# Performance work log

Hardware: AMD Instinct MI355X
Metric: run time of the kernel (lower is better)

Reference implementation:

```python
import jax, jax.numpy as jnp
import numpy as np

B, N, C = 4, 2048, 768
H = 12
DH = C // H
HID = int(C * 4.0)
SCALE = DH ** -0.5
EPS = 1e-5


def layernorm(x, g, b):
    mu = jnp.mean(x, axis=-1, keepdims=True)
    var = jnp.var(x, axis=-1, keepdims=True)
    return (x - mu) * jax.lax.rsqrt(var + EPS) * g + b


def setup_inputs() -> dict:
    key = jax.random.key(0)
    ks = jax.random.split(key, 10)
    s = lambda fan_in: 1.0 / np.sqrt(fan_in)
    return {
        "x": jax.random.normal(ks[0], (B, N, C), dtype=jnp.float32),
        "ln1_g": jnp.ones((C,), jnp.float32),
        "ln1_b": jnp.zeros((C,), jnp.float32),
        "w_qkv": jax.random.uniform(ks[1], (C, 3 * C), jnp.float32, -s(C), s(C)),
        "w_proj": jax.random.uniform(ks[2], (C, C), jnp.float32, -s(C), s(C)),
        "b_proj": jnp.zeros((C,), jnp.float32),
        "ln2_g": jnp.ones((C,), jnp.float32),
        "ln2_b": jnp.zeros((C,), jnp.float32),
        "w_fc1": jax.random.uniform(ks[3], (C, HID), jnp.float32, -s(C), s(C)),
        "b_fc1": jnp.zeros((HID,), jnp.float32),
        "w_fc2": jax.random.uniform(ks[4], (HID, C), jnp.float32, -s(HID), s(HID)),
        "b_fc2": jnp.zeros((C,), jnp.float32),
    }


def reference(x, ln1_g, ln1_b, w_qkv, w_proj, b_proj, ln2_g, ln2_b, w_fc1, b_fc1, w_fc2, b_fc2):
    # --- attention branch ---
    h = layernorm(x, ln1_g, ln1_b)                       # [B,N,C]
    qkv = (h @ w_qkv).reshape(B, N, 3, H, DH)
    q = qkv[:, :, 0].transpose(0, 2, 1, 3)               # [B,H,N,DH]
    k = qkv[:, :, 1].transpose(0, 2, 1, 3)
    v = qkv[:, :, 2].transpose(0, 2, 1, 3)
    attn = jnp.einsum('bhnd,bhmd->bhnm', q, k) * SCALE   # [B,H,N,N]
    attn = jax.nn.softmax(attn, axis=-1)
    y = jnp.einsum('bhnm,bhmd->bhnd', attn, v)           # [B,H,N,DH]
    y = y.transpose(0, 2, 1, 3).reshape(B, N, C)
    y = y @ w_proj + b_proj
    x = x + y
    # --- MLP branch ---
    h = layernorm(x, ln2_g, ln2_b)
    h = jax.nn.gelu(h @ w_fc1 + b_fc1, approximate=False)
    h = h @ w_fc2 + b_fc2
    return x + h
```

## Files before the change

kernel.cpp:

```cpp
#include <hip/hip_runtime.h>
#include <stdint.h>

#define DEV __device__ __forceinline__

typedef __attribute__((ext_vector_type(8))) short bf16x8;
typedef __attribute__((ext_vector_type(4))) float f32x4;
typedef __attribute__((ext_vector_type(4))) short s16x4;

DEV short f2bf(float f) {
    union { float f; unsigned u; } v; v.f = f;
    unsigned r = v.u + 0x7fffu + ((v.u >> 16) & 1u);
    return (short)(r >> 16);
}

DEV uint32_t cvtpk(float lo, float hi) {
    uint32_t r;
    asm("v_cvt_pk_bf16_f32 %0, %1, %2" : "=v"(r) : "v"(lo), "v"(hi));
    return r;
}

typedef const unsigned int __attribute__((address_space(1)))* gp1;
typedef unsigned int __attribute__((address_space(3)))* lp3;

DEV void gload16(const void* g, void* l) {
    __builtin_amdgcn_global_load_lds((gp1)g, (lp3)l, 16, 0, 0);
}

DEV void wait4_barrier() { asm volatile("s_waitcnt vmcnt(4)\ns_barrier" ::: "memory"); }
DEV void wait2_barrier() { asm volatile("s_waitcnt vmcnt(2)\ns_barrier" ::: "memory"); }
DEV void wait0_barrier() { asm volatile("s_waitcnt vmcnt(0)\ns_barrier" ::: "memory"); }

__global__ __launch_bounds__(256) void tcvt(
    const float* __restrict__ W, short* __restrict__ WT, int K, int N)
{
    __shared__ float t[32][33];
    int n0 = blockIdx.x * 32, k0 = blockIdx.y * 32;
    int tx = threadIdx.x & 31, ty = threadIdx.x >> 5;
#pragma unroll
    for (int i = 0; i < 32; i += 8)
        t[ty + i][tx] = W[(size_t)(k0 + ty + i) * N + n0 + tx];
    __syncthreads();
#pragma unroll
    for (int i = 0; i < 32; i += 8)
        WT[(size_t)(n0 + ty + i) * K + k0 + tx] = f2bf(t[tx][ty + i]);
}

__global__ __launch_bounds__(256) void ln_bf16(
    const float* __restrict__ x, const float* __restrict__ gam,
    const float* __restrict__ bet, short* __restrict__ out)
{
    const int w = threadIdx.x >> 6, lane = threadIdx.x & 63;
    const size_t row = (size_t)blockIdx.x * 4 + w;
    const float* xr = x + row * 768;
    float4 v[3];
    float s = 0.f, ss = 0.f;
#pragma unroll
    for (int k = 0; k < 3; ++k) {
        v[k] = *(const float4*)(xr + k * 256 + lane * 4);
        s  += v[k].x + v[k].y + v[k].z + v[k].w;
        ss += v[k].x * v[k].x + v[k].y * v[k].y + v[k].z * v[k].z + v[k].w * v[k].w;
    }
#pragma unroll
    for (int i = 1; i < 64; i <<= 1) { s += __shfl_xor(s, i, 64); ss += __shfl_xor(ss, i, 64); }
    const float inv = 1.f / 768.f;
    float mu = s * inv;
    float var = ss * inv - mu * mu;
    float rstd = rsqrtf(var + 1e-5f);
#pragma unroll
    for (int k = 0; k < 3; ++k) {
        int c = k * 256 + lane * 4;
        float vv[4] = { v[k].x, v[k].y, v[k].z, v[k].w };
        s16x4 o;
#pragma unroll
        for (int j = 0; j < 4; ++j)
            o[j] = f2bf((vv[j] - mu) * rstd * gam[c + j] + bet[c + j]);
        *(s16x4*)(out + row * 768 + c) = o;
    }
}

template<int MODE>
DEV void gemm_body(
    const short* __restrict__ A, const short* __restrict__ Bt,
    int M, int N, int K,
    const float* __restrict__ bias, const float* __restrict__ resid,
    float* __restrict__ outf, short* __restrict__ outb,
    short* __restrict__ qo, short* __restrict__ ko, short* __restrict__ vo,
    char* lds)
{
    const int tid = threadIdx.x;
    const int w = tid >> 6, lane = tid & 63;
    const int g = lane >> 4, l15 = lane & 15;
    const int brow = blockIdx.x * 128, bcol = blockIdx.y * 128;
    const int wr = w >> 1, wc = w & 1;
    f32x4 acc[4][4] = {};

    int aoff[4], boff[4];
#pragma unroll
    for (int m = 0; m < 4; ++m) {
        int ra = wr * 64 + m * 16 + l15;
        aoff[m] = ra * 64 + ((g * 16) ^ (((ra >> 1) & 3) << 4));
        int rb = wc * 64 + m * 16 + l15;
        boff[m] = 8192 + rb * 64 + ((g * 16) ^ (((rb >> 1) & 3) << 4));
    }
    int dA[2], dB[2];
    const char* pA[2]; const char* pB[2];
#pragma unroll
    for (int c = 0; c < 2; ++c) {
        int base = w * 2048 + c * 1024;
        int L = base + lane * 16;
        int r = L >> 6, b = L & 63;
        int bs = b ^ (((r >> 1) & 3) << 4);
        dA[c] = base; dB[c] = 8192 + base;
        pA[c] = (const char*)(A  + (size_t)(brow + r) * K) + bs;
        pB[c] = (const char*)(Bt + (size_t)(bcol + r) * K) + bs;
    }

#define GSTAGE(BUF, OFF) do { \
    gload16(pA[0] + (OFF), lds + (BUF) * 16384 + dA[0]); \
    gload16(pA[1] + (OFF), lds + (BUF) * 16384 + dA[1]); \
    gload16(pB[0] + (OFF), lds + (BUF) * 16384 + dB[0]); \
    gload16(pB[1] + (OFF), lds + (BUF) * 16384 + dB[1]); } while (0)

    const int KT = K >> 5;
    GSTAGE(0, 0);
    GSTAGE(1, 64);
    wait4_barrier();

    const int NM = KT / 3;
    for (int mi = 0; mi < NM; ++mi) {
#pragma unroll
        for (int u = 0; u < 3; ++u) {
            const int s = mi * 3 + u;
            if (s + 2 < KT) GSTAGE((u + 2) % 3, (u + 2) * 64);
            bf16x8 af[4], bfg[4];
#pragma unroll
            for (int m = 0; m < 4; ++m) {
                af[m]  = *(const bf16x8*)(lds + u * 16384 + aoff[m]);
                bfg[m] = *(const bf16x8*)(lds + u * 16384 + boff[m]);
            }
#pragma unroll
            for (int m = 0; m < 4; ++m)
#pragma unroll
                for (int n = 0; n < 4; ++n)
                    acc[m][n] = __builtin_amdgcn_mfma_f32_16x16x32_bf16(af[m], bfg[n], acc[m][n], 0, 0, 0);
            if (s + 1 < KT) {
                if (s + 2 < KT) wait4_barrier();
                else            wait0_barrier();
            }
        }
        pA[0] += 192; pA[1] += 192; pB[0] += 192; pB[1] += 192;
    }
#undef GSTAGE

#pragma unroll
    for (int m = 0; m < 4; ++m) {
#pragma unroll
        for (int n = 0; n < 4; ++n) {
#pragma unroll
            for (int j = 0; j < 4; ++j) {
                int r = brow + wr * 64 + m * 16 + g * 4 + j;
                int c = bcol + wc * 64 + n * 16 + l15;
                float v = acc[m][n][j];
                if (MODE == 0) {
                    int which = c / 768, cc = c % 768;
                    int h = cc >> 6, d = cc & 63;
                    int b_ = r >> 11, nn = r & 2047;
                    size_t bh = (size_t)b_ * 12 + h;
                    if (which == 0)      qo[(bh * 2048 + nn) * 64 + d] = f2bf(v * 0.18033688011112042f);
                    else if (which == 1) ko[(bh * 2048 + nn) * 64 + d] = f2bf(v);
                    else                 vo[(bh * 64 + d) * 2048 + nn] = f2bf(v);
                } else if (MODE == 1) {
                    outf[(size_t)r * N + c] = v + bias[c] + resid[(size_t)r * N + c];
                } else {
                    float t = v + bias[c];
                    float ge = 0.5f * t * (1.0f + erff(t * 0.70710678118654752f));
                    outb[(size_t)r * N + c] = f2bf(ge);
                }
            }
        }
    }
}

__global__ __launch_bounds__(256, 3) void g_qkv(
    const short* A, const short* Bt, int M, int N, int K,
    short* qo, short* ko, short* vo)
{
    __shared__ __align__(16) char lds[49152];
    gemm_body<0>(A, Bt, M, N, K, nullptr, nullptr, nullptr, nullptr, qo, ko, vo, lds);
}
__global__ __launch_bounds__(256, 3) void g_proj(
    const short* A, const short* Bt, int M, int N, int K,
    const float* bias, const float* resid, float* outf)
{
    __shared__ __align__(16) char lds[49152];
    gemm_body<1>(A, Bt, M, N, K, bias, resid, outf, nullptr, nullptr, nullptr, nullptr, lds);
}
__global__ __launch_bounds__(256, 3) void g_fc1(
    const short* A, const short* Bt, int M, int N, int K,
    const float* bias, short* outb)
{
    __shared__ __align__(16) char lds[49152];
    gemm_body<2>(A, Bt, M, N, K, bias, nullptr, nullptr, outb, nullptr, nullptr, nullptr, lds);
}
__global__ __launch_bounds__(256, 3) void g_fc2(
    const short* A, const short* Bt, int M, int N, int K,
    const float* bias, const float* resid, float* outf)
{
    __shared__ __align__(16) char lds[49152];
    gemm_body<1>(A, Bt, M, N, K, bias, resid, outf, nullptr, nullptr, nullptr, nullptr, lds);
}

__global__ __launch_bounds__(256, 3) void attn_fwd(
    const short* __restrict__ Q, const short* __restrict__ Kg,
    const short* __restrict__ Vt, short* __restrict__ Y)
{
    __shared__ __align__(16) char alds[40960];
    const int tid = threadIdx.x, w = tid >> 6, lane = tid & 63;
    const int g = lane >> 4, l15 = lane & 15;
    const int bh = blockIdx.y;
    const int q0 = blockIdx.x * 128 + w * 32;
    const short* Qb = Q  + (size_t)bh * 2048 * 64;
    const short* Kb = Kg + (size_t)bh * 2048 * 64;
    const short* Vb = Vt + (size_t)bh * 64 * 2048;

    bf16x8 qf[2][2];
#pragma unroll
    for (int m = 0; m < 2; ++m)
#pragma unroll
        for (int kk = 0; kk < 2; ++kk)
            qf[m][kk] = *(const bf16x8*)(Qb + (size_t)(q0 + m * 16 + l15) * 64 + kk * 32 + g * 8);

    f32x4 accO[2][4] = {};
    float lpart[2] = { 0.f, 0.f };

    int koff[2][2], voff[4], poff[2], pwoff[2][2];
#pragma unroll
    for (int n = 0; n < 2; ++n) {
        int key = n * 16 + l15;
#pragma unroll
        for (int kk = 0; kk < 2; ++kk)
            koff[kk][n] = key * 128 + ((kk * 64 + g * 16) ^ ((key & 7) << 4));
    }
#pragma unroll
    for (int n = 0; n < 4; ++n) {
        int d = n * 16 + l15;
        voff[n] = 16384 + d * 64 + ((g * 16) ^ (((d >> 1) & 3) << 4));
    }
#pragma unroll
    for (int m = 0; m < 2; ++m) {
        int qr = m * 16 + l15;
        int sw = ((qr >> 1) & 3) << 4;
        poff[m] = 32768 + w * 2048 + qr * 64 + ((g * 16) ^ sw);
#pragma unroll
        for (int n = 0; n < 2; ++n)
            pwoff[m][n] = 32768 + w * 2048 + qr * 64 + ((n * 32 + g * 8) ^ sw);
    }
    int dK, dV; const char* pK3; const char* pV3;
    {
        int bb = w * 1024;
        int L = bb + lane * 16;
        int rk = L >> 7, bk_ = L & 127;
        int bsk = bk_ ^ ((rk & 7) << 4);
        dK = bb;
        pK3 = (const char*)(Kb + (size_t)rk * 64) + bsk;
        int rv = L >> 6, bv = L & 63;
        int bsv = bv ^ (((rv >> 1) & 3) << 4);
        dV = bb;
        pV3 = (const char*)(Vb + (size_t)rv * 2048) + bsv;
    }
    gload16(pK3,        alds + dK);
    gload16(pV3,        alds + 16384 + dV);
    gload16(pK3 + 4096, alds + dK + 4096);
    gload16(pV3 + 64,   alds + 16384 + dV + 4096);
    gload16(pK3 + 8192, alds + dK + 8192);
    gload16(pV3 + 128,  alds + 16384 + dV + 8192);
    pK3 += 3 * 4096; pV3 += 3 * 64;
    wait4_barrier();

    for (int tm = 0; tm < 16; ++tm) {
#pragma unroll
        for (int tu = 0; tu < 4; ++tu) {
            const int t = tm * 4 + tu;
            if (t + 3 < 64) {
                gload16(pK3, alds + dK + ((tu + 3) & 3) * 4096);
                gload16(pV3, alds + 16384 + dV + ((tu + 3) & 3) * 4096);
                pK3 += 4096; pV3 += 64;
            }

            f32x4 s2[2][2] = {};
            __builtin_amdgcn_s_setprio(1);
#pragma unroll
            for (int kk = 0; kk < 2; ++kk) {
                bf16x8 kf[2];
#pragma unroll
                for (int n = 0; n < 2; ++n)
                    kf[n] = *(const bf16x8*)(alds + tu * 4096 + koff[kk][n]);
#pragma unroll
                for (int m = 0; m < 2; ++m)
#pragma unroll
                    for (int n = 0; n < 2; ++n)
                        s2[m][n] = __builtin_amdgcn_mfma_f32_16x16x32_bf16(kf[n], qf[m][kk], s2[m][n], 0, 0, 0);
            }
            __builtin_amdgcn_s_setprio(0);

#pragma unroll
            for (int m = 0; m < 2; ++m)
#pragma unroll
                for (int n = 0; n < 2; ++n) {
                    float e0 = __builtin_amdgcn_exp2f(s2[m][n][0]);
                    float e1 = __builtin_amdgcn_exp2f(s2[m][n][1]);
                    float e2 = __builtin_amdgcn_exp2f(s2[m][n][2]);
                    float e3 = __builtin_amdgcn_exp2f(s2[m][n][3]);
                    lpart[m] += (e0 + e1) + (e2 + e3);
                    uint2 pk; pk.x = cvtpk(e0, e1); pk.y = cvtpk(e2, e3);
                    *(uint2*)(alds + pwoff[m][n]) = pk;
                }

            __builtin_amdgcn_s_setprio(1);
            {
                bf16x8 vf[4], pf[2];
#pragma unroll
                for (int n = 0; n < 4; ++n)
                    vf[n] = *(const bf16x8*)(alds + tu * 4096 + voff[n]);
#pragma unroll
                for (int m = 0; m < 2; ++m)
                    pf[m] = *(const bf16x8*)(alds + poff[m]);
#pragma unroll
                for (int m = 0; m < 2; ++m)
#pragma unroll
                    for (int n = 0; n < 4; ++n)
                        accO[m][n] = __builtin_amdgcn_mfma_f32_16x16x32_bf16(pf[m], vf[n], accO[m][n], 0, 0, 0);
            }
            __builtin_amdgcn_s_setprio(0);

            if (t < 61)       wait4_barrier();
            else if (t == 61) wait2_barrier();
            else if (t == 62) wait0_barrier();
        }
    }

#pragma unroll
    for (int m = 0; m < 2; ++m) {
        lpart[m] += __shfl_xor(lpart[m], 16, 64);
        lpart[m] += __shfl_xor(lpart[m], 32, 64);
    }

    int b_ = bh / 12, h = bh % 12;
#pragma unroll
    for (int m = 0; m < 2; ++m) {
        float linv[4];
#pragma unroll
        for (int j = 0; j < 4; ++j)
            linv[j] = 1.0f / __shfl(lpart[m], g * 4 + j, 64);
#pragma unroll
        for (int n = 0; n < 4; ++n)
#pragma unroll
            for (int j = 0; j < 4; ++j) {
                int qq = q0 + m * 16 + g * 4 + j;
                int d = n * 16 + l15;
                Y[((size_t)b_ * 2048 + qq) * 768 + h * 64 + d] = f2bf(accO[m][n][j] * linv[j]);
            }
    }
}

extern "C" void kernel_launch(void* const* d_in, const int* in_sizes, int n_in,
                              void* d_out, int out_size, void* d_ws, size_t ws_size,
                              hipStream_t stream)
{
    const float* x      = (const float*)d_in[0];
    const float* ln1_g  = (const float*)d_in[1];
    const float* ln1_b  = (const float*)d_in[2];
    const float* w_qkv  = (const float*)d_in[3];
    const float* w_proj = (const float*)d_in[4];
    const float* b_proj = (const float*)d_in[5];
    const float* ln2_g  = (const float*)d_in[6];
    const float* ln2_b  = (const float*)d_in[7];
    const float* w_fc1  = (const float*)d_in[8];
    const float* b_fc1  = (const float*)d_in[9];
    const float* w_fc2  = (const float*)d_in[10];
    const float* b_fc2  = (const float*)d_in[11];

    char* ws = (char*)d_ws;
    size_t off = 0;
    auto alloc = [&](size_t bytes) -> void* {
        void* p = ws + off; off += (bytes + 255) & ~(size_t)255; return p;
    };
    short* wqkvT = (short*)alloc((size_t)2304 * 768 * 2);
    short* wprojT= (short*)alloc((size_t)768 * 768 * 2);
    short* wfc1T = (short*)alloc((size_t)3072 * 768 * 2);
    short* wfc2T = (short*)alloc((size_t)768 * 3072 * 2);
    short* h1    = (short*)alloc((size_t)8192 * 768 * 2);
    short* qb    = (short*)alloc((size_t)48 * 2048 * 64 * 2);
    short* kb    = (short*)alloc((size_t)48 * 2048 * 64 * 2);
    short* vtb   = (short*)alloc((size_t)48 * 64 * 2048 * 2);
    short* yb    = (short*)alloc((size_t)8192 * 768 * 2);
    float* X1    = (float*)alloc((size_t)8192 * 768 * 4);
    short* h2    = (short*)alloc((size_t)8192 * 768 * 2);
    short* h3    = (short*)alloc((size_t)8192 * 3072 * 2);

    tcvt<<<dim3(2304 / 32, 768 / 32),  256, 0, stream>>>(w_qkv,  wqkvT,  768,  2304);
    tcvt<<<dim3(768 / 32,  768 / 32),  256, 0, stream>>>(w_proj, wprojT, 768,  768);
    tcvt<<<dim3(3072 / 32, 768 / 32),  256, 0, stream>>>(w_fc1,  wfc1T,  768,  3072);
    tcvt<<<dim3(768 / 32,  3072 / 32), 256, 0, stream>>>(w_fc2,  wfc2T,  3072, 768);

    ln_bf16<<<2048, 256, 0, stream>>>(x, ln1_g, ln1_b, h1);

    g_qkv<<<dim3(64, 18), 256, 0, stream>>>(h1, wqkvT, 8192, 2304, 768, qb, kb, vtb);

    attn_fwd<<<dim3(16, 48), 256, 0, stream>>>(qb, kb, vtb, yb);

    g_proj<<<dim3(64, 6), 256, 0, stream>>>(yb, wprojT, 8192, 768, 768, b_proj, x, X1);

    ln_bf16<<<2048, 256, 0, stream>>>(X1, ln2_g, ln2_b, h2);

    g_fc1<<<dim3(64, 24), 256, 0, stream>>>(h2, wfc1T, 8192, 3072, 768, b_fc1, h3);

    g_fc2<<<dim3(64, 6), 256, 0, stream>>>(h3, wfc2T, 8192, 768, 3072, b_fc2, X1, (float*)d_out);
}
```

Baseline: 274.6 us.

## Load GEMM MFMA fragments directly from global memory, dropping LDS staging

The GEMM body no longer stages A and B tiles through a triple-buffered, swizzled LDS ring with barriers. Each wave now loads its own bf16x8 operand fragments straight from global memory into registers, double-buffered across K steps. This removes the LDS traffic and workgroup barriers, but the two waves sharing a row or column band each fetch it separately, so global/L2 reads roughly double. Each load is also only 16 bytes per row, which coalesces worse than the old 64-byte row chunks.

```diff
diff --git a/kernel.cpp b/kernel.cpp
--- a/kernel.cpp
+++ b/kernel.cpp
@@ -84,8 +84,7 @@
     int M, int N, int K,
     const float* __restrict__ bias, const float* __restrict__ resid,
     float* __restrict__ outf, short* __restrict__ outb,
-    short* __restrict__ qo, short* __restrict__ ko, short* __restrict__ vo,
-    char* lds)
+    short* __restrict__ qo, short* __restrict__ ko, short* __restrict__ vo)
 {
     const int tid = threadIdx.x;
     const int w = tid >> 6, lane = tid & 63;
@@ -94,63 +93,40 @@
     const int wr = w >> 1, wc = w & 1;
     f32x4 acc[4][4] = {};
 
-    int aoff[4], boff[4];
+    const char* pA[4];
+    const char* pB[4];
 #pragma unroll
     for (int m = 0; m < 4; ++m) {
-        int ra = wr * 64 + m * 16 + l15;
-        aoff[m] = ra * 64 + ((g * 16) ^ (((ra >> 1) & 3) << 4));
-        int rb = wc * 64 + m * 16 + l15;
-        boff[m] = 8192 + rb * 64 + ((g * 16) ^ (((rb >> 1) & 3) << 4));
-    }
-    int dA[2], dB[2];
-    const char* pA[2]; const char* pB[2];
-#pragma unroll
-    for (int c = 0; c < 2; ++c) {
-        int base = w * 2048 + c * 1024;
-        int L = base + lane * 16;
-        int r = L >> 6, b = L & 63;
-        int bs = b ^ (((r >> 1) & 3) << 4);
-        dA[c] = base; dB[c] = 8192 + base;
-        pA[c] = (const char*)(A  + (size_t)(brow + r) * K) + bs;
-        pB[c] = (const char*)(Bt + (size_t)(bcol + r) * K) + bs;
-    }
-
-#define GSTAGE(BUF, OFF) do { \
-    gload16(pA[0] + (OFF), lds + (BUF) * 16384 + dA[0]); \
-    gload16(pA[1] + (OFF), lds + (BUF) * 16384 + dA[1]); \
-    gload16(pB[0] + (OFF), lds + (BUF) * 16384 + dB[0]); \
-    gload16(pB[1] + (OFF), lds + (BUF) * 16384 + dB[1]); } while (0)
+        pA[m] = (const char*)(A  + (size_t)(brow + wr * 64 + m * 16 + l15) * K) + g * 16;
+        pB[m] = (const char*)(Bt + (size_t)(bcol + wc * 64 + m * 16 + l15) * K) + g * 16;
+    }
+
+    bf16x8 a0[4], b0[4], a1[4], b1[4];
+#define LDF(AS, BS, OFF) do {                          \
+    _Pragma("unroll")                                  \
+    for (int m = 0; m < 4; ++m) {                      \
+        AS[m] = *(const bf16x8*)(pA[m] + (OFF));       \
+        BS[m] = *(const bf16x8*)(pB[m] + (OFF));       \
+    } } while (0)
+#define MM(AS, BS) do {                                \
+    _Pragma("unroll")                                  \
+    for (int m = 0; m < 4; ++m)                        \
+        _Pragma("unroll")                              \
+        for (int n = 0; n < 4; ++n)                    \
+            acc[m][n] = __builtin_amdgcn_mfma_f32_16x16x32_bf16(AS[m], BS[n], acc[m][n], 0, 0, 0); \
+    } while (0)
 
     const int KT = K >> 5;
-    GSTAGE(0, 0);
-    GSTAGE(1, 64);
-    wait4_barrier();
-
-    const int NM = KT / 3;
-    for (int mi = 0; mi < NM; ++mi) {
-#pragma unroll
-        for (int u = 0; u < 3; ++u) {
-            const int s = mi * 3 + u;
-            if (s + 2 < KT) GSTAGE((u + 2) % 3, (u + 2) * 64);
-            bf16x8 af[4], bfg[4];
-#pragma unroll
-            for (int m = 0; m < 4; ++m) {
-                af[m]  = *(const bf16x8*)(lds + u * 16384 + aoff[m]);
-                bfg[m] = *(const bf16x8*)(lds + u * 16384 + boff[m]);
-            }
-#pragma unroll
-            for (int m = 0; m < 4; ++m)
-#pragma unroll
-                for (int n = 0; n < 4; ++n)
-                    acc[m][n] = __builtin_amdgcn_mfma_f32_16x16x32_bf16(af[m], bfg[n], acc[m][n], 0, 0, 0);
-            if (s + 1 < KT) {
-                if (s + 2 < KT) wait4_barrier();
-                else            wait0_barrier();
-            }
-        }
-        pA[0] += 192; pA[1] += 192; pB[0] += 192; pB[1] += 192;
-    }
-#undef GSTAGE
+    LDF(a0, b0, 0);
+    LDF(a1, b1, 64);
+    for (int s = 0; s < KT; s += 2) {
+        MM(a0, b0);
+        if (s + 2 < KT) LDF(a0, b0, (s + 2) * 64);
+        MM(a1, b1);
+        if (s + 3 < KT) LDF(a1, b1, (s + 3) * 64);
+    }
+#undef LDF
+#undef MM
 
 #pragma unroll
     for (int m = 0; m < 4; ++m) {
@@ -185,29 +161,25 @@
     const short* A, const short* Bt, int M, int N, int K,
     short* qo, short* ko, short* vo)
 {
-    __shared__ __align__(16) char lds[49152];
-    gemm_body<0>(A, Bt, M, N, K, nullptr, nullptr, nullptr, nullptr, qo, ko, vo, lds);
+    gemm_body<0>(A, Bt, M, N, K, nullptr, nullptr, nullptr, nullptr, qo, ko, vo);
 }
 __global__ __launch_bounds__(256, 3) void g_proj(
     const short* A, const short* Bt, int M, int N, int K,
     const float* bias, const float* resid, float* outf)
 {
-    __shared__ __align__(16) char lds[49152];
-    gemm_body<1>(A, Bt, M, N, K, bias, resid, outf, nullptr, nullptr, nullptr, nullptr, lds);
+    gemm_body<1>(A, Bt, M, N, K, bias, resid, outf, nullptr, nullptr, nullptr, nullptr);
 }
 __global__ __launch_bounds__(256, 3) void g_fc1(
     const short* A, const short* Bt, int M, int N, int K,
     const float* bias, short* outb)
 {
-    __shared__ __align__(16) char lds[49152];
-    gemm_body<2>(A, Bt, M, N, K, bias, nullptr, nullptr, outb, nullptr, nullptr, nullptr, lds);
+    gemm_body<2>(A, Bt, M, N, K, bias, nullptr, nullptr, outb, nullptr, nullptr, nullptr);
 }
 __global__ __launch_bounds__(256, 3) void g_fc2(
     const short* A, const short* Bt, int M, int N, int K,
     const float* bias, const float* resid, float* outf)
 {
-    __shared__ __align__(16) char lds[49152];
-    gemm_body<1>(A, Bt, M, N, K, bias, resid, outf, nullptr, nullptr, nullptr, nullptr, lds);
+    gemm_body<1>(A, Bt, M, N, K, bias, resid, outf, nullptr, nullptr, nullptr, nullptr);
 }
 
 __global__ __launch_bounds__(256, 3) void attn_fwd(
```

Result: slower. 568.4 us (+107.0%).

## Split-K the proj and fc2 GEMMs with atomic fp32 accumulation

Applied to the files above, without the earlier changes.

The projection GEMM is split into 2 K-slices and the fc2 GEMM into 4 K-slices along a third grid dimension. Partial results are accumulated into fp32 outputs with atomicAdd, and only the first slice adds bias and residual. The aim is to fill more CUs than the 384-block grids did before. In exchange it adds two full-size memsets, atomic write traffic and a nondeterministic summation order.

```diff
diff --git a/kernel.cpp b/kernel.cpp
--- a/kernel.cpp
+++ b/kernel.cpp
@@ -78,10 +78,10 @@
     }
 }
 
-template<int MODE>
+template<int MODE, bool ATOMIC>
 DEV void gemm_body(
     const short* __restrict__ A, const short* __restrict__ Bt,
-    int M, int N, int K,
+    int M, int N, int Kfull, int k0, int klen,
     const float* __restrict__ bias, const float* __restrict__ resid,
     float* __restrict__ outf, short* __restrict__ outb,
     short* __restrict__ qo, short* __restrict__ ko, short* __restrict__ vo,
@@ -111,8 +111,8 @@
         int r = L >> 6, b = L & 63;
         int bs = b ^ (((r >> 1) & 3) << 4);
         dA[c] = base; dB[c] = 8192 + base;
-        pA[c] = (const char*)(A  + (size_t)(brow + r) * K) + bs;
-        pB[c] = (const char*)(Bt + (size_t)(bcol + r) * K) + bs;
+        pA[c] = (const char*)(A  + (size_t)(brow + r) * Kfull + k0) + bs;
+        pB[c] = (const char*)(Bt + (size_t)(bcol + r) * Kfull + k0) + bs;
     }
 
 #define GSTAGE(BUF, OFF) do { \
@@ -121,7 +121,7 @@
     gload16(pB[0] + (OFF), lds + (BUF) * 16384 + dB[0]); \
     gload16(pB[1] + (OFF), lds + (BUF) * 16384 + dB[1]); } while (0)
 
-    const int KT = K >> 5;
+    const int KT = klen >> 5;
     GSTAGE(0, 0);
     GSTAGE(1, 64);
     wait4_barrier();
@@ -170,7 +170,13 @@
                     else if (which == 1) ko[(bh * 2048 + nn) * 64 + d] = f2bf(v);
                     else                 vo[(bh * 64 + d) * 2048 + nn] = f2bf(v);
                 } else if (MODE == 1) {
-                    outf[(size_t)r * N + c] = v + bias[c] + resid[(size_t)r * N + c];
+                    if (ATOMIC) {
+                        float add = v;
+                        if (k0 == 0) add += bias[c] + resid[(size_t)r * N + c];
+                        atomicAdd(&outf[(size_t)r * N + c], add);
+                    } else {
+                        outf[(size_t)r * N + c] = v + bias[c] + resid[(size_t)r * N + c];
+                    }
                 } else {
                     float t = v + bias[c];
                     float ge = 0.5f * t * (1.0f + erff(t * 0.70710678118654752f));
@@ -186,28 +192,30 @@
     short* qo, short* ko, short* vo)
 {
     __shared__ __align__(16) char lds[49152];
-    gemm_body<0>(A, Bt, M, N, K, nullptr, nullptr, nullptr, nullptr, qo, ko, vo, lds);
+    gemm_body<0, false>(A, Bt, M, N, K, 0, K, nullptr, nullptr, nullptr, nullptr, qo, ko, vo, lds);
 }
 __global__ __launch_bounds__(256, 3) void g_proj(
-    const short* A, const short* Bt, int M, int N, int K,
+    const short* A, const short* Bt, int M, int N, int K, int klen,
     const float* bias, const float* resid, float* outf)
 {
     __shared__ __align__(16) char lds[49152];
-    gemm_body<1>(A, Bt, M, N, K, bias, resid, outf, nullptr, nullptr, nullptr, nullptr, lds);
+    gemm_body<1, true>(A, Bt, M, N, K, blockIdx.z * klen, klen,
+                       bias, resid, outf, nullptr, nullptr, nullptr, nullptr, lds);
 }
 __global__ __launch_bounds__(256, 3) void g_fc1(
     const short* A, const short* Bt, int M, int N, int K,
     const float* bias, short* outb)
 {
     __shared__ __align__(16) char lds[49152];
-    gemm_body<2>(A, Bt, M, N, K, bias, nullptr, nullptr, outb, nullptr, nullptr, nullptr, lds);
+    gemm_body<2, false>(A, Bt, M, N, K, 0, K, bias, nullptr, nullptr, outb, nullptr, nullptr, nullptr, lds);
 }
 __global__ __launch_bounds__(256, 3) void g_fc2(
-    const short* A, const short* Bt, int M, int N, int K,
+    const short* A, const short* Bt, int M, int N, int K, int klen,
     const float* bias, const float* resid, float* outf)
 {
     __shared__ __align__(16) char lds[49152];
-    gemm_body<1>(A, Bt, M, N, K, bias, resid, outf, nullptr, nullptr, nullptr, nullptr, lds);
+    gemm_body<1, true>(A, Bt, M, N, K, blockIdx.z * klen, klen,
+                       bias, resid, outf, nullptr, nullptr, nullptr, nullptr, lds);
 }
 
 __global__ __launch_bounds__(256, 3) void attn_fwd(
@@ -398,6 +406,9 @@
     short* h2    = (short*)alloc((size_t)8192 * 768 * 2);
     short* h3    = (short*)alloc((size_t)8192 * 3072 * 2);
 
+    hipMemsetAsync(X1, 0, (size_t)8192 * 768 * 4, stream);
+    hipMemsetAsync(d_out, 0, (size_t)8192 * 768 * 4, stream);
+
     tcvt<<<dim3(2304 / 32, 768 / 32),  256, 0, stream>>>(w_qkv,  wqkvT,  768,  2304);
     tcvt<<<dim3(768 / 32,  768 / 32),  256, 0, stream>>>(w_proj, wprojT, 768,  768);
     tcvt<<<dim3(3072 / 32, 768 / 32),  256, 0, stream>>>(w_fc1,  wfc1T,  768,  3072);
@@ -409,11 +420,13 @@
 
     attn_fwd<<<dim3(16, 48), 256, 0, stream>>>(qb, kb, vtb, yb);
 
-    g_proj<<<dim3(64, 6), 256, 0, stream>>>(yb, wprojT, 8192, 768, 768, b_proj, x, X1);
+    g_proj<<<dim3(64, 6, 2), 256, 0, stream>>>(yb, wprojT, 8192, 768, 768, 384,
+        b_proj, x, X1);
 
     ln_bf16<<<2048, 256, 0, stream>>>(X1, ln2_g, ln2_b, h2);
 
     g_fc1<<<dim3(64, 24), 256, 0, stream>>>(h2, wfc1T, 8192, 3072, 768, b_fc1, h3);
 
-    g_fc2<<<dim3(64, 6), 256, 0, stream>>>(h3, wfc2T, 8192, 768, 3072, b_fc2, X1, (float*)d_out);
-}
+    g_fc2<<<dim3(64, 6, 4), 256, 0, stream>>>(h3, wfc2T, 8192, 768, 3072, 768,
+        b_fc2, X1, (float*)d_out);
+}
```

After: 364.8 us. +32.8%, slower.

## Use eight waves per GEMM block with 64x32 per-wave subtiles

Applied to the files above, without the earlier changes.

Doubles the GEMM block to 512 threads and splits the 128x128 output tile into eight 64x32 wave subtiles instead of four 64x64 ones. Each thread now issues one A and one B 16-byte load per stage instead of two each, and the wait counts are adjusted to match. The intent is more resident waves to hide memory and LDS latency, with fewer accumulator registers per thread. The cost is a lower MFMA-to-LDS-read ratio per wave and more barrier participants.

```diff
diff --git a/kernel.cpp b/kernel.cpp
--- a/kernel.cpp
+++ b/kernel.cpp
@@ -91,40 +91,37 @@
     const int w = tid >> 6, lane = tid & 63;
     const int g = lane >> 4, l15 = lane & 15;
     const int brow = blockIdx.x * 128, bcol = blockIdx.y * 128;
-    const int wr = w >> 1, wc = w & 1;
-    f32x4 acc[4][4] = {};
-
-    int aoff[4], boff[4];
+    const int wr = w >> 2, wc = w & 3;
+    f32x4 acc[4][2] = {};
+
+    int aoff[4], boff[2];
 #pragma unroll
     for (int m = 0; m < 4; ++m) {
         int ra = wr * 64 + m * 16 + l15;
         aoff[m] = ra * 64 + ((g * 16) ^ (((ra >> 1) & 3) << 4));
-        int rb = wc * 64 + m * 16 + l15;
-        boff[m] = 8192 + rb * 64 + ((g * 16) ^ (((rb >> 1) & 3) << 4));
-    }
-    int dA[2], dB[2];
-    const char* pA[2]; const char* pB[2];
-#pragma unroll
-    for (int c = 0; c < 2; ++c) {
-        int base = w * 2048 + c * 1024;
-        int L = base + lane * 16;
-        int r = L >> 6, b = L & 63;
+    }
+#pragma unroll
+    for (int n = 0; n < 2; ++n) {
+        int rb = wc * 32 + n * 16 + l15;
+        boff[n] = 8192 + rb * 64 + ((g * 16) ^ (((rb >> 1) & 3) << 4));
+    }
+    const int dStage = tid * 16;
+    const char* pA; const char* pB;
+    {
+        int r = dStage >> 6, b = dStage & 63;
         int bs = b ^ (((r >> 1) & 3) << 4);
-        dA[c] = base; dB[c] = 8192 + base;
-        pA[c] = (const char*)(A  + (size_t)(brow + r) * K) + bs;
-        pB[c] = (const char*)(Bt + (size_t)(bcol + r) * K) + bs;
+        pA = (const char*)(A  + (size_t)(brow + r) * K) + bs;
+        pB = (const char*)(Bt + (size_t)(bcol + r) * K) + bs;
     }
 
 #define GSTAGE(BUF, OFF) do { \
-    gload16(pA[0] + (OFF), lds + (BUF) * 16384 + dA[0]); \
-    gload16(pA[1] + (OFF), lds + (BUF) * 16384 + dA[1]); \
-    gload16(pB[0] + (OFF), lds + (BUF) * 16384 + dB[0]); \
-    gload16(pB[1] + (OFF), lds + (BUF) * 16384 + dB[1]); } while (0)
+    gload16(pA + (OFF), lds + (BUF) * 16384 + dStage); \
+    gload16(pB + (OFF), lds + (BUF) * 16384 + 8192 + dStage); } while (0)
 
     const int KT = K >> 5;
     GSTAGE(0, 0);
     GSTAGE(1, 64);
-    wait4_barrier();
+    wait2_barrier();
 
     const int NM = KT / 3;
     for (int mi = 0; mi < NM; ++mi) {
@@ -132,34 +129,35 @@
         for (int u = 0; u < 3; ++u) {
             const int s = mi * 3 + u;
             if (s + 2 < KT) GSTAGE((u + 2) % 3, (u + 2) * 64);
-            bf16x8 af[4], bfg[4];
-#pragma unroll
-            for (int m = 0; m < 4; ++m) {
+            bf16x8 af[4], bfg[2];
+#pragma unroll
+            for (int m = 0; m < 4; ++m)
                 af[m]  = *(const bf16x8*)(lds + u * 16384 + aoff[m]);
-                bfg[m] = *(const bf16x8*)(lds + u * 16384 + boff[m]);
-            }
+#pragma unroll
+            for (int n = 0; n < 2; ++n)
+                bfg[n] = *(const bf16x8*)(lds + u * 16384 + boff[n]);
 #pragma unroll
             for (int m = 0; m < 4; ++m)
 #pragma unroll
-                for (int n = 0; n < 4; ++n)
+                for (int n = 0; n < 2; ++n)
                     acc[m][n] = __builtin_amdgcn_mfma_f32_16x16x32_bf16(af[m], bfg[n], acc[m][n], 0, 0, 0);
             if (s + 1 < KT) {
-                if (s + 2 < KT) wait4_barrier();
+                if (s + 2 < KT) wait2_barrier();
                 else            wait0_barrier();
             }
         }
-        pA[0] += 192; pA[1] += 192; pB[0] += 192; pB[1] += 192;
+        pA += 192; pB += 192;
     }
 #undef GSTAGE
 
 #pragma unroll
     for (int m = 0; m < 4; ++m) {
 #pragma unroll
-        for (int n = 0; n < 4; ++n) {
+        for (int n = 0; n < 2; ++n) {
 #pragma unroll
             for (int j = 0; j < 4; ++j) {
                 int r = brow + wr * 64 + m * 16 + g * 4 + j;
-                int c = bcol + wc * 64 + n * 16 + l15;
+                int c = bcol + wc * 32 + n * 16 + l15;
                 float v = acc[m][n][j];
                 if (MODE == 0) {
                     int which = c / 768, cc = c % 768;
@@ -181,28 +179,28 @@
     }
 }
 
-__global__ __launch_bounds__(256, 3) void g_qkv(
+__global__ __launch_bounds__(512, 6) void g_qkv(
     const short* A, const short* Bt, int M, int N, int K,
     short* qo, short* ko, short* vo)
 {
     __shared__ __align__(16) char lds[49152];
     gemm_body<0>(A, Bt, M, N, K, nullptr, nullptr, nullptr, nullptr, qo, ko, vo, lds);
 }
-__global__ __launch_bounds__(256, 3) void g_proj(
+__global__ __launch_bounds__(512, 6) void g_proj(
     const short* A, const short* Bt, int M, int N, int K,
     const float* bias, const float* resid, float* outf)
 {
     __shared__ __align__(16) char lds[49152];
     gemm_body<1>(A, Bt, M, N, K, bias, resid, outf, nullptr, nullptr, nullptr, nullptr, lds);
 }
-__global__ __launch_bounds__(256, 3) void g_fc1(
+__global__ __launch_bounds__(512, 6) void g_fc1(
     const short* A, const short* Bt, int M, int N, int K,
     const float* bias, short* outb)
 {
     __shared__ __align__(16) char lds[49152];
     gemm_body<2>(A, Bt, M, N, K, bias, nullptr, nullptr, outb, nullptr, nullptr, nullptr, lds);
 }
-__global__ __launch_bounds__(256, 3) void g_fc2(
+__global__ __launch_bounds__(512, 6) void g_fc2(
     const short* A, const short* Bt, int M, int N, int K,
     const float* bias, const float* resid, float* outf)
 {
@@ -405,15 +403,15 @@
 
     ln_bf16<<<2048, 256, 0, stream>>>(x, ln1_g, ln1_b, h1);
 
-    g_qkv<<<dim3(64, 18), 256, 0, stream>>>(h1, wqkvT, 8192, 2304, 768, qb, kb, vtb);
+    g_qkv<<<dim3(64, 18), 512, 0, stream>>>(h1, wqkvT, 8192, 2304, 768, qb, kb, vtb);
 
     attn_fwd<<<dim3(16, 48), 256, 0, stream>>>(qb, kb, vtb, yb);
 
-    g_proj<<<dim3(64, 6), 256, 0, stream>>>(yb, wprojT, 8192, 768, 768, b_proj, x, X1);
+    g_proj<<<dim3(64, 6), 512, 0, stream>>>(yb, wprojT, 8192, 768, 768, b_proj, x, X1);
 
     ln_bf16<<<2048, 256, 0, stream>>>(X1, ln2_g, ln2_b, h2);
 
-    g_fc1<<<dim3(64, 24), 256, 0, stream>>>(h2, wfc1T, 8192, 3072, 768, b_fc1, h3);
-
-    g_fc2<<<dim3(64, 6), 256, 0, stream>>>(h3, wfc2T, 8192, 768, 3072, b_fc2, X1, (float*)d_out);
-}
+    g_fc1<<<dim3(64, 24), 512, 0, stream>>>(h2, wfc1T, 8192, 3072, 768, b_fc1, h3);
+
+    g_fc2<<<dim3(64, 6), 512, 0, stream>>>(h3, wfc2T, 8192, 768, 3072, b_fc2, X1, (float*)d_out);
+}
```

After: 270.9 us. About the same (-1.4%).
